# Kernel tuning notes

Measured on AMD Instinct MI355X. Metric: run time of the kernel, lower is better.

The kernel has to match this reference:

```python
import jax, jax.numpy as jnp
import numpy as np

NUM_GROUPS = 8
INPUT_DIM = 1024
OUTPUT_DIM = 1024
TOKENS_PER_GROUP = 8192  # rows per group after reshape


def setup_inputs() -> dict:
    key = jax.random.key(0)
    kx, kw = jax.random.split(key)
    # x: [N*G, D_in] as fed to the torch module (it reshapes internally)
    x = jax.random.normal(kx, (TOKENS_PER_GROUP * NUM_GROUPS, INPUT_DIM), dtype=jnp.float32)
    # Stacked per-group Linear weights, torch layout [D_out, D_in] per group.
    # Xavier-normal gain=1: std = sqrt(2 / (fan_in + fan_out))
    std = np.sqrt(2.0 / (INPUT_DIM + OUTPUT_DIM)).astype(np.float32)
    W = jax.random.normal(kw, (NUM_GROUPS, OUTPUT_DIM, INPUT_DIM), dtype=jnp.float32) * std
    return {"x": x, "W": W}


def reference(x, W):
    # x: [N*G, D_in] -> [N, G, D_in]
    n = x.shape[0] // NUM_GROUPS
    xg = x.reshape(n, NUM_GROUPS, INPUT_DIM)
    # per-group linear: out[n,g,k] = sum_d xg[n,g,d] * W[g,k,d]
    out = jnp.einsum("ngd,gkd->ngk", xg, W)
    return out.reshape(-1, OUTPUT_DIM)
```

## Files before the change

kernel.cpp:

```cpp
#include <hip/hip_runtime.h>
#include <hip/hip_bf16.h>


namespace {

constexpr int NG   = 8;
constexpr int DIN  = 1024;
constexpr int DOUT = 1024;
constexpr int BM   = 256;
constexpr int BN   = 256;
constexpr int BK   = 64;
constexpr int NKT  = DIN / BK;
constexpr int ROWB = BK * 2;
constexpr int TILE = BM * ROWB;
constexpr int LDS_BYTES = 4 * TILE;
constexpr int JTN  = DOUT / BN;

typedef __attribute__((ext_vector_type(8))) short bf16x8;
typedef __attribute__((ext_vector_type(4))) float f32x4;

__device__ __forceinline__ bf16x8 pack_bf16x8v(f32x4 lo, f32x4 hi) {
  union { __hip_bfloat162 h2[4]; bf16x8 v; } p;
  p.h2[0] = __float22bfloat162_rn(make_float2(lo.x, lo.y));
  p.h2[1] = __float22bfloat162_rn(make_float2(lo.z, lo.w));
  p.h2[2] = __float22bfloat162_rn(make_float2(hi.x, hi.y));
  p.h2[3] = __float22bfloat162_rn(make_float2(hi.z, hi.w));
  return p.v;
}

#define FENCE() asm volatile("" ::: "memory")
#define BAR()   do { FENCE(); __builtin_amdgcn_s_barrier(); FENCE(); } while (0)
#define LGKM0() asm volatile("s_waitcnt lgkmcnt(0)" ::: "memory")
#define MFMA_(a, b, c) __builtin_amdgcn_mfma_f32_16x16x32_bf16((a), (b), (c), 0, 0, 0)

__device__ __forceinline__ void stage_tile(
    const float* __restrict__ aB, const float* __restrict__ bB, int kcol,
    char* __restrict__ nA, char* __restrict__ nB, int pdst0) {
  f32x4 aL[16], bL[16];
#pragma unroll
  for (int j = 0; j < 8; ++j) {
    const float* s = aB + (size_t)j * (32 * NG * DIN) + kcol;
    aL[2 * j]     = *(const f32x4*)(s);
    aL[2 * j + 1] = *(const f32x4*)(s + 4);
  }
#pragma unroll
  for (int j = 0; j < 8; ++j) {
    const float* s = bB + (size_t)j * (32 * DIN) + kcol;
    bL[2 * j]     = *(const f32x4*)(s);
    bL[2 * j + 1] = *(const f32x4*)(s + 4);
  }
#pragma unroll
  for (int j = 0; j < 8; ++j)
    *(bf16x8*)(nA + pdst0 + j * 4096) = pack_bf16x8v(aL[2 * j], aL[2 * j + 1]);
#pragma unroll
  for (int j = 0; j < 8; ++j)
    *(bf16x8*)(nB + pdst0 + j * 4096) = pack_bf16x8v(bL[2 * j], bL[2 * j + 1]);
}

__global__ __launch_bounds__(768)
void gemm_spec(const float* __restrict__ X, const float* __restrict__ W,
               float* __restrict__ O) {
  extern __shared__ char smem[];
  char* const smA = smem;
  char* const smB = smem + 2 * TILE;

  const int bid = (int)blockIdx.x;
  const int swz = (bid & 7) * 128 + (bid >> 3);
  const int jt = swz & 3;
  const int it = (swz >> 2) & 31;
  const int g  = swz >> 7;

  const int n0 = it * BM;
  const int c0 = jt * BN;

  const int tid  = (int)threadIdx.x;
  const int lane = tid & 63;
  const int wid  = tid >> 6;

  const int ptid = tid - 512;
  const int prow = (ptid & 255) >> 3;
  const int pchk = ptid & 7;
  const float* aB = X + ((size_t)(n0 + prow) * NG + g) * DIN + pchk * 8;
  const float* bB = W + ((size_t)(g * DOUT + c0 + prow)) * DIN + pchk * 8;
  const int pdst0 = prow * ROWB + ((pchk ^ (prow & 7)) << 4);

  const int wr = (wid >> 2) & 1;
  const int wc = wid & 3;
  const int fr = lane & 15;
  const int fq = lane >> 4;
  const int colx0 = ((fq     ^ (fr & 7)) << 4);
  const int colx1 = (((4 + fq) ^ (fr & 7)) << 4);
  const int aRow0 = (wr * 128 + fr) * ROWB;
  const int bRow0 = (wc * 64  + fr) * ROWB;

  if (wid >= 8) {
    stage_tile(aB, bB, 0, smA, smB, pdst0);
    LGKM0();
  }
  BAR();

  if (wid < 8) {
    f32x4 acc[8][4];
#pragma unroll
    for (int m = 0; m < 8; ++m)
#pragma unroll
      for (int n = 0; n < 4; ++n) acc[m][n] = (f32x4){0.f, 0.f, 0.f, 0.f};

    for (int t = 0; t < NKT; ++t) {
      char* const cA = smA + (t & 1) * TILE;
      char* const cB = smB + (t & 1) * TILE;
#pragma unroll
      for (int ks = 0; ks < 2; ++ks) {
        const int cx = ks ? colx1 : colx0;
        bf16x8 bfr[4];
#pragma unroll
        for (int n = 0; n < 4; ++n)
          bfr[n] = *(const bf16x8*)(cB + bRow0 + n * 2048 + cx);
        __builtin_amdgcn_s_setprio(1);
#pragma unroll
        for (int m = 0; m < 8; ++m) {
          bf16x8 am = *(const bf16x8*)(cA + aRow0 + m * 2048 + cx);
#pragma unroll
          for (int n = 0; n < 4; ++n)
            acc[m][n] = MFMA_(am, bfr[n], acc[m][n]);
        }
        __builtin_amdgcn_s_setprio(0);
      }
      if (t + 1 < NKT) BAR();
    }

#pragma unroll
    for (int m = 0; m < 8; ++m) {
#pragma unroll
      for (int r = 0; r < 4; ++r) {
        const int row = wr * 128 + m * 16 + fq * 4 + r;
        float* orow = O + ((size_t)(n0 + row) * NG + g) * DOUT + c0 + wc * 64;
#pragma unroll
        for (int n = 0; n < 4; ++n) {
          orow[n * 16 + fr] = acc[m][n][r];
        }
      }
    }
  } else {
    for (int t = 0; t + 1 < NKT; ++t) {
      char* const nA = smA + ((t + 1) & 1) * TILE;
      char* const nB = smB + ((t + 1) & 1) * TILE;
      stage_tile(aB, bB, (t + 1) * BK, nA, nB, pdst0);
      LGKM0();
      BAR();
    }
  }
}

}

extern "C" void kernel_launch(void* const* d_in, const int* in_sizes, int n_in,
                              void* d_out, int out_size, void* d_ws, size_t ws_size,
                              hipStream_t stream) {
  (void)n_in; (void)d_ws; (void)ws_size; (void)out_size;
  const float* X = (const float*)d_in[0];
  const float* W = (const float*)d_in[1];
  float* O = (float*)d_out;

  const int tokens_total = in_sizes[0] / DIN;
  const int ntok_per_g   = tokens_total / NG;
  const int grid = NG * (ntok_per_g / BM) * (DOUT / BN);

  (void)hipFuncSetAttribute((const void*)gemm_spec,
                            hipFuncAttributeMaxDynamicSharedMemorySize,
                            LDS_BYTES);
  gemm_spec<<<dim3(grid), dim3(768), LDS_BYTES, stream>>>(X, W, O);
}
```

Measured before the change: 223.7 us.

## Pre-convert W to swizzled bf16 tiles and stream them into LDS directly

Adds a pre-pass kernel that converts W to bf16 in the pre-swizzled per-tile LDS layout inside the workspace. The GEMM producer warps then copy B tiles with global_load_lds directly into shared memory. The producer group grows from 4 to 8 warps (1024 threads), and A loads are software-pipelined two tiles ahead using vmcnt waits. The aim is to halve B global traffic, drop the fp32-to-bf16 conversion from the main loop, and hide load latency better. The cost is an extra kernel launch plus workspace traffic, and more register pressure from the larger block.

```diff
diff --git a/kernel.cpp b/kernel.cpp
--- a/kernel.cpp
+++ b/kernel.cpp
@@ -15,6 +15,7 @@
 constexpr int TILE = BM * ROWB;
 constexpr int LDS_BYTES = 4 * TILE;
 constexpr int JTN  = DOUT / BN;
+constexpr size_t WSB_BYTES = (size_t)NG * JTN * NKT * TILE;
 
 typedef __attribute__((ext_vector_type(8))) short bf16x8;
 typedef __attribute__((ext_vector_type(4))) float f32x4;
@@ -28,38 +29,93 @@
   return p.v;
 }
 
+__device__ __forceinline__ void glds16(const void* g, void* l) {
+  __builtin_amdgcn_global_load_lds(
+      (const __attribute__((address_space(1))) unsigned int*)g,
+      (__attribute__((address_space(3))) unsigned int*)l, 16, 0, 0);
+}
+
 #define FENCE() asm volatile("" ::: "memory")
 #define BAR()   do { FENCE(); __builtin_amdgcn_s_barrier(); FENCE(); } while (0)
 #define LGKM0() asm volatile("s_waitcnt lgkmcnt(0)" ::: "memory")
+#define VM0()   asm volatile("s_waitcnt vmcnt(0)" ::: "memory")
+#define VMC8()  asm volatile("s_waitcnt vmcnt(8)" ::: "memory")
 #define MFMA_(a, b, c) __builtin_amdgcn_mfma_f32_16x16x32_bf16((a), (b), (c), 0, 0, 0)
 
-__device__ __forceinline__ void stage_tile(
-    const float* __restrict__ aB, const float* __restrict__ bB, int kcol,
-    char* __restrict__ nA, char* __restrict__ nB, int pdst0) {
-  f32x4 aL[16], bL[16];
-#pragma unroll
-  for (int j = 0; j < 8; ++j) {
-    const float* s = aB + (size_t)j * (32 * NG * DIN) + kcol;
-    aL[2 * j]     = *(const f32x4*)(s);
-    aL[2 * j + 1] = *(const f32x4*)(s + 4);
+__global__ __launch_bounds__(256)
+void cvt_w_kernel(const float* __restrict__ W, char* __restrict__ wsB) {
+  const int q    = (int)blockIdx.x * 256 + (int)threadIdx.x;
+  const int tile = q >> 13;
+  const int q13  = q & 8191;
+  const int r    = q13 >> 5;
+  const int cp   = q13 & 31;
+  const int g    = tile >> 6;
+  const int jt   = (tile >> 4) & 3;
+  const int kt   = tile & 15;
+
+  const float2 s = *(const float2*)(
+      W + ((size_t)(g * DOUT + jt * BN + r)) * DIN + kt * 64 + 2 * cp);
+  union { __hip_bfloat162 h; unsigned u; } pk;
+  pk.h = __float22bfloat162_rn(make_float2(s.x, s.y));
+
+  const int swzr = (r & 7) << 4;
+  const int dstByte = r * ROWB + (((cp >> 2) * 16) ^ swzr) + (cp & 3) * 4;
+  *(unsigned*)(wsB + (size_t)tile * TILE + dstByte) = pk.u;
+}
+
+#define ISSUE_A(TT, CUR)                                                       \
+  { const float* Ai = aSrc + (size_t)(TT) * BK;                                \
+    _Pragma("unroll")                                                          \
+    for (int p = 0; p < 4; ++p) {                                              \
+      aS[CUR][2 * p]     = *(const f32x4*)(Ai + p * ARSTR);                    \
+      aS[CUR][2 * p + 1] = *(const f32x4*)(Ai + p * ARSTR + 4);                \
+    } }
+
+#define ISSUE_B(TT, DBUF)                                                      \
+  { if (WSB) {                                                                 \
+      const char* Bi = BgT + (size_t)(TT) * TILE;                              \
+      _Pragma("unroll")                                                        \
+      for (int p = 0; p < 4; ++p)                                              \
+        glds16(Bi + dst0 + p * 8192, (DBUF) + dst0 + p * 8192);                \
+    } else {                                                                   \
+      const float* Bi = bSrc + (size_t)(TT) * BK;                              \
+      _Pragma("unroll")                                                        \
+      for (int p = 0; p < 4; ++p) {                                            \
+        bS[2 * p]     = *(const f32x4*)(Bi + p * BRSTR);                       \
+        bS[2 * p + 1] = *(const f32x4*)(Bi + p * BRSTR + 4);                   \
+      } } }
+
+#define WRITE_A(CUR, DBUF)                                                     \
+  { _Pragma("unroll")                                                          \
+    for (int p = 0; p < 4; ++p)                                                \
+      *(bf16x8*)((DBUF) + dst0 + p * 8192) =                                   \
+          pack_bf16x8v(aS[CUR][2 * p], aS[CUR][2 * p + 1]); }
+
+#define WRITE_B(DBUF)                                                          \
+  { _Pragma("unroll")                                                          \
+    for (int p = 0; p < 4; ++p)                                                \
+      *(bf16x8*)((DBUF) + dst0 + p * 8192) =                                   \
+          pack_bf16x8v(bS[2 * p], bS[2 * p + 1]); }
+
+#define PBODY(T, CUR)                                                          \
+  {                                                                            \
+    char* const nA = smA + (((T) + 1) & 1) * TILE;                             \
+    char* const nB = smB + (((T) + 1) & 1) * TILE;                             \
+    ISSUE_B((T) + 1, nB);                                                      \
+    const bool st2 = (T) + 2 < NKT;                                            \
+    if (st2) ISSUE_A((T) + 2, CUR);                                            \
+    FENCE();                                                                   \
+    if (st2) { VMC8(); } else { VM0(); }                                       \
+    WRITE_A((CUR) ^ 1, nA);                                                    \
+    if (!WSB) WRITE_B(nB);                                                     \
+    LGKM0();                                                                   \
+    BAR();                                                                     \
   }
-#pragma unroll
-  for (int j = 0; j < 8; ++j) {
-    const float* s = bB + (size_t)j * (32 * DIN) + kcol;
-    bL[2 * j]     = *(const f32x4*)(s);
-    bL[2 * j + 1] = *(const f32x4*)(s + 4);
-  }
-#pragma unroll
-  for (int j = 0; j < 8; ++j)
-    *(bf16x8*)(nA + pdst0 + j * 4096) = pack_bf16x8v(aL[2 * j], aL[2 * j + 1]);
-#pragma unroll
-  for (int j = 0; j < 8; ++j)
-    *(bf16x8*)(nB + pdst0 + j * 4096) = pack_bf16x8v(bL[2 * j], bL[2 * j + 1]);
-}
-
-__global__ __launch_bounds__(768)
-void gemm_spec(const float* __restrict__ X, const float* __restrict__ W,
-               float* __restrict__ O) {
+
+template <bool WSB>
+__global__ __launch_bounds__(1024)
+void gemm_ws(const float* __restrict__ X, const float* __restrict__ W,
+             const char* __restrict__ wsB, float* __restrict__ O) {
   extern __shared__ char smem[];
   char* const smA = smem;
   char* const smB = smem + 2 * TILE;
@@ -77,34 +133,23 @@
   const int lane = tid & 63;
   const int wid  = tid >> 6;
 
-  const int ptid = tid - 512;
-  const int prow = (ptid & 255) >> 3;
-  const int pchk = ptid & 7;
-  const float* aB = X + ((size_t)(n0 + prow) * NG + g) * DIN + pchk * 8;
-  const float* bB = W + ((size_t)(g * DOUT + c0 + prow)) * DIN + pchk * 8;
-  const int pdst0 = prow * ROWB + ((pchk ^ (prow & 7)) << 4);
-
-  const int wr = (wid >> 2) & 1;
-  const int wc = wid & 3;
-  const int fr = lane & 15;
-  const int fq = lane >> 4;
-  const int colx0 = ((fq     ^ (fr & 7)) << 4);
-  const int colx1 = (((4 + fq) ^ (fr & 7)) << 4);
-  const int aRow0 = (wr * 128 + fr) * ROWB;
-  const int bRow0 = (wc * 64  + fr) * ROWB;
-
-  if (wid >= 8) {
-    stage_tile(aB, bB, 0, smA, smB, pdst0);
-    LGKM0();
-  }
-  BAR();
-
   if (wid < 8) {
+    const int wr = (wid >> 2) & 1;
+    const int wc = wid & 3;
+    const int fr = lane & 15;
+    const int fq = lane >> 4;
+    const int colx0 = ((fq       ^ (fr & 7)) << 4);
+    const int colx1 = (((4 + fq) ^ (fr & 7)) << 4);
+    const int aRow0 = (wr * 128 + fr) * ROWB;
+    const int bRow0 = (wc * 64  + fr) * ROWB;
+
     f32x4 acc[8][4];
 #pragma unroll
     for (int m = 0; m < 8; ++m)
 #pragma unroll
       for (int n = 0; n < 4; ++n) acc[m][n] = (f32x4){0.f, 0.f, 0.f, 0.f};
+
+    BAR();
 
     for (int t = 0; t < NKT; ++t) {
       char* const cA = smA + (t & 1) * TILE;
@@ -142,12 +187,34 @@
       }
     }
   } else {
-    for (int t = 0; t + 1 < NKT; ++t) {
-      char* const nA = smA + ((t + 1) & 1) * TILE;
-      char* const nB = smB + ((t + 1) & 1) * TILE;
-      stage_tile(aB, bB, (t + 1) * BK, nA, nB, pdst0);
-      LGKM0();
-      BAR();
+    const int ptid = tid - 512;
+    const int r0   = ptid >> 3;
+    const int sl   = ptid & 7;
+    const int lg   = sl ^ (r0 & 7);
+    const int dst0 = ptid * 16;
+
+    const float* aSrc = X + ((size_t)(n0 + r0) * NG + g) * DIN + lg * 8;
+    constexpr size_t ARSTR = (size_t)64 * NG * DIN;
+    const char* BgT = wsB + (size_t)((g * JTN + jt) * NKT) * TILE;
+    const float* bSrc = W + ((size_t)(g * DOUT + c0 + r0)) * DIN + lg * 8;
+    constexpr size_t BRSTR = (size_t)64 * DIN;
+
+    f32x4 aS[2][8];
+    f32x4 bS[8];
+
+    ISSUE_B(0, smB);
+    ISSUE_A(0, 0);
+    ISSUE_A(1, 1);
+    FENCE();
+    VMC8();
+    WRITE_A(0, smA);
+    if (!WSB) WRITE_B(smB);
+    LGKM0();
+    BAR();
+
+    for (int tt = 0; tt < NKT - 1; tt += 2) {
+      PBODY(tt, 0);
+      if (tt + 1 < NKT - 1) PBODY(tt + 1, 1);
     }
   }
 }
@@ -157,7 +224,7 @@
 extern "C" void kernel_launch(void* const* d_in, const int* in_sizes, int n_in,
                               void* d_out, int out_size, void* d_ws, size_t ws_size,
                               hipStream_t stream) {
-  (void)n_in; (void)d_ws; (void)ws_size; (void)out_size;
+  (void)n_in; (void)out_size;
   const float* X = (const float*)d_in[0];
   const float* W = (const float*)d_in[1];
   float* O = (float*)d_out;
@@ -166,8 +233,19 @@
   const int ntok_per_g   = tokens_total / NG;
   const int grid = NG * (ntok_per_g / BM) * (DOUT / BN);
 
-  (void)hipFuncSetAttribute((const void*)gemm_spec,
-                            hipFuncAttributeMaxDynamicSharedMemorySize,
-                            LDS_BYTES);
-  gemm_spec<<<dim3(grid), dim3(768), LDS_BYTES, stream>>>(X, W, O);
-}
+  if (ws_size >= WSB_BYTES) {
+    const int cvt_grid = (int)(WSB_BYTES / 4 / 256);
+    cvt_w_kernel<<<dim3(cvt_grid), dim3(256), 0, stream>>>(W, (char*)d_ws);
+    (void)hipFuncSetAttribute((const void*)gemm_ws<true>,
+                              hipFuncAttributeMaxDynamicSharedMemorySize,
+                              LDS_BYTES);
+    gemm_ws<true><<<dim3(grid), dim3(1024), LDS_BYTES, stream>>>(
+        X, W, (const char*)d_ws, O);
+  } else {
+    (void)hipFuncSetAttribute((const void*)gemm_ws<false>,
+                              hipFuncAttributeMaxDynamicSharedMemorySize,
+                              LDS_BYTES);
+    gemm_ws<false><<<dim3(grid), dim3(1024), LDS_BYTES, stream>>>(
+        X, W, nullptr, O);
+  }
+}
```

Result: slower. 763.2 us (+241.1%).
